# Kernel optimization log

Measured on AMD Instinct MI355X. Metric: run time of the kernel, lower is better.

Reference implementation:

```python
import jax, jax.numpy as jnp
import numpy as np


def setup_inputs() -> dict:
    key = jax.random.key(0)
    k1, k2 = jax.random.split(key)
    B, H, W = 32, 512, 512
    F, KH, KW = 32, 3, 3
    x = jax.random.normal(k1, (B, H, W), dtype=jnp.float32)
    # TF TruncatedNormal(mean=0.5, stddev=0.05 default)
    kernel_w = 0.5 + 0.05 * jax.random.truncated_normal(k2, -2.0, 2.0, (F, KH, KW), dtype=jnp.float32)
    biases = jnp.zeros((F,), dtype=jnp.float32)
    return {"x": x, "kernel_w": kernel_w, "biases": biases}


def reference(x, kernel_w, biases):
    # Quantize inputs and weights (binarized/ternary-style)
    x_q = jnp.round(x)                                   # [B,H,W]
    k_q = jnp.clip(jnp.round(kernel_w), -1.0, 1.0)       # [F,KH,KW]
    # scipy convolve2d is true convolution -> flip kernel spatially
    k_flip = k_q[:, ::-1, ::-1]
    # [F,KH,KW] -> HWIO [KH,KW,1,F]
    w = jnp.transpose(k_flip, (1, 2, 0))[:, :, None, :]
    xb = x_q[..., None]                                  # NHWC with C=1
    out = jax.lax.conv_general_dilated(
        xb, w, window_strides=(1, 1), padding='VALID',
        dimension_numbers=('NHWC', 'HWIO', 'NHWC'))      # [B,H-2,W-2,F]
    out = out + jnp.round(biases)                        # rounded per-channel bias
    # training-phase activation (binarization >=0 is the inference branch)
    return jax.nn.relu(out)
```

## Files before the change

### kernel.cpp

```cpp
#include <hip/hip_runtime.h>


#define BATCH 32
#define H 512
#define W 512
#define NF 32
#define HO 510
#define WO 510

__global__ __launch_bounds__(256) void cwt_conv_kernel(
    const float* __restrict__ x,
    const float* __restrict__ kw,
    const float* __restrict__ bias,
    float* __restrict__ out,
    int total4, int nthreads)
{
    int g = blockIdx.x * blockDim.x + threadIdx.x;
    int f4 = g & 7;

    float wq[9][4];
    float bq[4];
#pragma unroll
    for (int c = 0; c < 4; ++c) {
        int f = f4 * 4 + c;
#pragma unroll
        for (int t = 0; t < 9; ++t) {
            float v = rintf(kw[f * 9 + (8 - t)]);
            v = fminf(fmaxf(v, -1.0f), 1.0f);
            wq[t][c] = v;
        }
        bq[c] = rintf(bias[f]);
    }

    for (int idx4 = g; idx4 < total4; idx4 += nthreads) {
        int s  = idx4 >> 3;
        int j  = s % WO;
        int t2 = s / WO;
        int i  = t2 % HO;
        int b  = t2 / HO;
        const float* xp = x + ((size_t)(b * H + i) * W + j);

        float acc0 = bq[0], acc1 = bq[1], acc2 = bq[2], acc3 = bq[3];
#pragma unroll
        for (int di = 0; di < 3; ++di) {
#pragma unroll
            for (int dj = 0; dj < 3; ++dj) {
                float xv = rintf(xp[di * W + dj]);
                int t = di * 3 + dj;
                acc0 = fmaf(xv, wq[t][0], acc0);
                acc1 = fmaf(xv, wq[t][1], acc1);
                acc2 = fmaf(xv, wq[t][2], acc2);
                acc3 = fmaf(xv, wq[t][3], acc3);
            }
        }
        float4 r;
        r.x = fmaxf(acc0, 0.0f);
        r.y = fmaxf(acc1, 0.0f);
        r.z = fmaxf(acc2, 0.0f);
        r.w = fmaxf(acc3, 0.0f);
        reinterpret_cast<float4*>(out)[idx4] = r;
    }
}

extern "C" void kernel_launch(void* const* d_in, const int* in_sizes, int n_in,
                              void* d_out, int out_size, void* d_ws, size_t ws_size,
                              hipStream_t stream) {
    const float* x    = (const float*)d_in[0];
    const float* kw   = (const float*)d_in[1];
    const float* bias = (const float*)d_in[2];
    float* out = (float*)d_out;

    constexpr int total4 = BATCH * HO * WO * (NF / 4);
    const int block = 256;
    const int grid  = 4096;
    cwt_conv_kernel<<<grid, block, 0, stream>>>(x, kw, bias, out, total4, grid * block);
}
```

Baseline: 1.198 ms.

## Map threads to 2D output tiles with register-blocked 4-column input reuse

Replaces the grid-stride flat loop with a 3D grid (column tile, output row, batch), so each thread computes 4 adjacent output columns for 4 filters. The 3x6 input window is loaded once with vector float4/float2 loads and rounded once, instead of issuing 9 scalar loads and roundings per output. This also removes the per-element div/mod index decoding. In exchange the kernel uses more registers, and it needs edge guards for the last column tile.

```diff
diff --git a/kernel.cpp b/kernel.cpp
--- a/kernel.cpp
+++ b/kernel.cpp
@@ -12,11 +12,14 @@
     const float* __restrict__ x,
     const float* __restrict__ kw,
     const float* __restrict__ bias,
-    float* __restrict__ out,
-    int total4, int nthreads)
+    float* __restrict__ out)
 {
-    int g = blockIdx.x * blockDim.x + threadIdx.x;
-    int f4 = g & 7;
+    const int tid = threadIdx.x;
+    const int f4  = tid & 7;
+    const int jq  = tid >> 3;
+    const int i   = blockIdx.y;
+    const int b   = blockIdx.z;
+    const int j0  = blockIdx.x * 128 + jq * 4;
 
     float wq[9][4];
     float bq[4];
@@ -26,39 +29,58 @@
 #pragma unroll
         for (int t = 0; t < 9; ++t) {
             float v = rintf(kw[f * 9 + (8 - t)]);
-            v = fminf(fmaxf(v, -1.0f), 1.0f);
-            wq[t][c] = v;
+            wq[t][c] = fminf(fmaxf(v, -1.0f), 1.0f);
         }
         bq[c] = rintf(bias[f]);
     }
 
-    for (int idx4 = g; idx4 < total4; idx4 += nthreads) {
-        int s  = idx4 >> 3;
-        int j  = s % WO;
-        int t2 = s / WO;
-        int i  = t2 % HO;
-        int b  = t2 / HO;
-        const float* xp = x + ((size_t)(b * H + i) * W + j);
+    const float* rp = x + ((size_t)(b * H + i) * W + j0);
+    const bool have6 = (j0 <= W - 8);
+    float xr[3][6];
+#pragma unroll
+    for (int r = 0; r < 3; ++r) {
+        const float4 v4 = *reinterpret_cast<const float4*>(rp + (size_t)r * W);
+        xr[r][0] = rintf(v4.x);
+        xr[r][1] = rintf(v4.y);
+        xr[r][2] = rintf(v4.z);
+        xr[r][3] = rintf(v4.w);
+        if (have6) {
+            const float2 v2 = *reinterpret_cast<const float2*>(rp + (size_t)r * W + 4);
+            xr[r][4] = rintf(v2.x);
+            xr[r][5] = rintf(v2.y);
+        } else {
+            xr[r][4] = 0.0f;
+            xr[r][5] = 0.0f;
+        }
+    }
 
-        float acc0 = bq[0], acc1 = bq[1], acc2 = bq[2], acc3 = bq[3];
+    float4* out4 = reinterpret_cast<float4*>(out);
+    const int obase = ((b * HO + i) * WO + j0) * (NF / 4) + f4;
+
 #pragma unroll
-        for (int di = 0; di < 3; ++di) {
+    for (int jj = 0; jj < 4; ++jj) {
+        const int j = j0 + jj;
+        float a0 = bq[0], a1 = bq[1], a2 = bq[2], a3 = bq[3];
+#pragma unroll
+        for (int r = 0; r < 3; ++r) {
 #pragma unroll
             for (int dj = 0; dj < 3; ++dj) {
-                float xv = rintf(xp[di * W + dj]);
-                int t = di * 3 + dj;
-                acc0 = fmaf(xv, wq[t][0], acc0);
-                acc1 = fmaf(xv, wq[t][1], acc1);
-                acc2 = fmaf(xv, wq[t][2], acc2);
-                acc3 = fmaf(xv, wq[t][3], acc3);
+                const float xv = xr[r][jj + dj];
+                const int t = r * 3 + dj;
+                a0 = fmaf(xv, wq[t][0], a0);
+                a1 = fmaf(xv, wq[t][1], a1);
+                a2 = fmaf(xv, wq[t][2], a2);
+                a3 = fmaf(xv, wq[t][3], a3);
             }
         }
-        float4 r;
-        r.x = fmaxf(acc0, 0.0f);
-        r.y = fmaxf(acc1, 0.0f);
-        r.z = fmaxf(acc2, 0.0f);
-        r.w = fmaxf(acc3, 0.0f);
-        reinterpret_cast<float4*>(out)[idx4] = r;
+        if (j < WO) {
+            float4 o;
+            o.x = fmaxf(a0, 0.0f);
+            o.y = fmaxf(a1, 0.0f);
+            o.z = fmaxf(a2, 0.0f);
+            o.w = fmaxf(a3, 0.0f);
+            out4[obase + jj * (NF / 4)] = o;
+        }
     }
 }
 
@@ -70,8 +92,7 @@
     const float* bias = (const float*)d_in[2];
     float* out = (float*)d_out;
 
-    constexpr int total4 = BATCH * HO * WO * (NF / 4);
-    const int block = 256;
-    const int grid  = 4096;
-    cwt_conv_kernel<<<grid, block, 0, stream>>>(x, kw, bias, out, total4, grid * block);
+    dim3 grid(4, HO, BATCH);
+    dim3 block(256);
+    cwt_conv_kernel<<<grid, block, 0, stream>>>(x, kw, bias, out);
 }
```

New measurement: 1.204 ms. No clear change (+0.5%).
